# Performance work log

Hardware: AMD Instinct MI355X
Metric: run time of the kernel (lower is better)

## Reference

```python
import jax, jax.numpy as jnp
import numpy as np

SPATIAL_SHAPES = ((80, 80), (40, 40), (20, 20))  # strides 8/16/32 on 640x640
NUM_HEADS = 8
N_POINTS = 4
D_MODEL = 256
OFFSET_SCALE = 0.5
N_LEVELS = len(SPATIAL_SHAPES)
TOTAL_P = N_LEVELS * N_POINTS


def setup_inputs() -> dict:
    key = jax.random.key(0)
    ks = jax.random.split(key, 11)
    B, Q = 32, 300
    S = sum(h * w for h, w in SPATIAL_SHAPES)  # 8400
    d = D_MODEL
    s = 0.02
    return {
        "hidden_states": jax.random.normal(ks[0], (B, Q, d), jnp.float32),
        "encoder_hidden_states": jax.random.normal(ks[1], (B, S, d), jnp.float32),
        "reference_points": jax.random.uniform(ks[2], (B, Q, 1, 4), jnp.float32, 0.1, 0.9),
        "W_off": jax.random.normal(ks[3], (d, NUM_HEADS * TOTAL_P * 2), jnp.float32) * s,
        "b_off": jax.random.normal(ks[4], (NUM_HEADS * TOTAL_P * 2,), jnp.float32) * s,
        "W_attn": jax.random.normal(ks[5], (d, NUM_HEADS * TOTAL_P), jnp.float32) * s,
        "b_attn": jax.random.normal(ks[6], (NUM_HEADS * TOTAL_P,), jnp.float32) * s,
        "W_val": jax.random.normal(ks[7], (d, d), jnp.float32) * s,
        "b_val": jax.random.normal(ks[8], (d,), jnp.float32) * s,
        "W_out": jax.random.normal(ks[9], (d, d), jnp.float32) * s,
        "b_out": jax.random.normal(ks[10], (d,), jnp.float32) * s,
    }


def _bilinear_sample(img, grid):
    # img: (N, H, W, C); grid: (N, Q, P, 2), normalized coords in [-1, 1]
    # torch grid_sample(mode='bilinear', padding_mode='zeros', align_corners=False)
    N, Hh, Ww, C = img.shape
    gx = (grid[..., 0] + 1.0) * (Ww * 0.5) - 0.5
    gy = (grid[..., 1] + 1.0) * (Hh * 0.5) - 0.5
    x0 = jnp.floor(gx)
    y0 = jnp.floor(gy)
    wx1 = gx - x0
    wx0 = 1.0 - wx1
    wy1 = gy - y0
    wy0 = 1.0 - wy1
    n_idx = jnp.arange(N)[:, None, None]

    def tap(ix, iy, w):
        valid = (ix >= 0) & (ix < Ww) & (iy >= 0) & (iy < Hh)
        ixc = jnp.clip(ix, 0, Ww - 1).astype(jnp.int32)
        iyc = jnp.clip(iy, 0, Hh - 1).astype(jnp.int32)
        v = img[n_idx, iyc, ixc]  # (N, Q, P, C)
        return v * (w * valid.astype(w.dtype))[..., None]

    return (tap(x0, y0, wx0 * wy0) + tap(x0 + 1.0, y0, wx1 * wy0)
            + tap(x0, y0 + 1.0, wx0 * wy1) + tap(x0 + 1.0, y0 + 1.0, wx1 * wy1))


def reference(hidden_states, encoder_hidden_states, reference_points,
              W_off, b_off, W_attn, b_attn, W_val, b_val, W_out, b_out):
    B, Q, d = hidden_states.shape
    S = encoder_hidden_states.shape[1]
    H = NUM_HEADS
    C = d // H

    value = (encoder_hidden_states @ W_val + b_val).reshape(B, S, H, C)
    offs = (hidden_states @ W_off + b_off).reshape(B, Q, H, TOTAL_P, 2)
    attn = jax.nn.softmax((hidden_states @ W_attn + b_attn).reshape(B, Q, H, TOTAL_P), axis=-1)

    # 4-d reference points branch (boxes): loc = ref_xy + off * (1/P) * ref_wh * offset_scale
    n_points_scale = jnp.full((TOTAL_P, 1), 1.0 / N_POINTS, hidden_states.dtype)
    loc = (reference_points[:, :, None, :, :2]
           + offs * n_points_scale * reference_points[:, :, None, :, 2:] * OFFSET_SCALE)
    grids = 2.0 * loc - 1.0  # method='default'
    grids = grids.transpose(0, 2, 1, 3, 4).reshape(B * H, Q, TOTAL_P, 2)

    value_bh = value.transpose(0, 2, 1, 3).reshape(B * H, S, C)

    samples = []
    start = 0
    p0 = 0
    for (h, w) in SPATIAL_SHAPES:
        v_l = value_bh[:, start:start + h * w].reshape(B * H, h, w, C)
        g_l = grids[:, :, p0:p0 + N_POINTS]
        samples.append(_bilinear_sample(v_l, g_l))
        start += h * w
        p0 += N_POINTS
    sampled = jnp.concatenate(samples, axis=2)  # (B*H, Q, TOTAL_P, C)

    attn_bh = attn.transpose(0, 2, 1, 3).reshape(B * H, Q, TOTAL_P)
    out = jnp.einsum("nqpc,nqp->nqc", sampled, attn_bh)  # (B*H, Q, C)
    out = out.reshape(B, H, Q, C).transpose(0, 2, 1, 3).reshape(B, Q, H * C)
    return out @ W_out + b_out
```

## Files before the change

### kernel.cpp

```cpp
#include <hip/hip_runtime.h>
#include <hip/hip_fp16.h>

#define DEVI __device__ __forceinline__

typedef _Float16 f16x8 __attribute__((ext_vector_type(8)));
typedef float f32x4 __attribute__((ext_vector_type(4)));

static DEVI unsigned short f2h_u(float f) {
    _Float16 h = (_Float16)f;
    return __builtin_bit_cast(unsigned short, h);
}
static DEVI float h2f_u(unsigned short u) {
    return (float)__builtin_bit_cast(_Float16, u);
}
static DEVI unsigned pk2(float a, float b) {
    return (unsigned)f2h_u(a) | ((unsigned)f2h_u(b) << 16);
}


__global__ __launch_bounds__(256) void prep_weights(
    const float* __restrict__ W_val, const float* __restrict__ W_off,
    const float* __restrict__ W_attn, const float* __restrict__ W_out,
    const float* __restrict__ b_off, const float* __restrict__ b_attn,
    unsigned short* __restrict__ Wst, unsigned short* __restrict__ Wct,
    unsigned short* __restrict__ Wot, float* __restrict__ cbias)
{
    int idx = blockIdx.x * 256 + threadIdx.x;
    if (idx < 65536) {
        int n = idx >> 8, k = idx & 255;
        Wst[(((n >> 7) * 32 + (k >> 3)) * 128 + (n & 127)) * 8 + (k & 7)] =
            f2h_u(W_val[k * 256 + n]);
    } else if (idx < 65536 + 73728) {
        int j = idx - 65536;
        int n = j >> 8, k = j & 255;
        Wct[j] = f2h_u(n < 192 ? W_off[k * 192 + n] : W_attn[k * 96 + (n - 192)]);
    } else if (idx < 204800) {
        int j = idx - 139264;
        int n = j >> 8, k = j & 255;
        Wot[j] = f2h_u(W_out[k * 256 + n]);
    } else if (idx < 205088) {
        int j = idx - 204800;
        cbias[j] = (j < 192) ? b_off[j] : b_attn[j - 192];
    }
}

__global__ __launch_bounds__(256, 2) void gemm_value(
    const float* __restrict__ A, const unsigned short* __restrict__ Wst,
    const float* __restrict__ bias, unsigned short* __restrict__ out)
{
    __shared__ __align__(16) unsigned short Bs[32 * 128 * 8];
    const int tid  = threadIdx.x;
    const int wave = tid >> 6;
    const int lane = tid & 63;
    const int l15  = lane & 15;
    const int qd   = lane >> 4;
    const size_t m0 = (size_t)blockIdx.x * 64;

#pragma unroll
    for (int it = 0; it < 16; ++it) {
        const int c = wave * 16 + it;
        const unsigned short* gp = Wst + c * 512 + lane * 8;
        unsigned short* lp = Bs + c * 512;
        __builtin_amdgcn_global_load_lds(
            (const __attribute__((address_space(1))) void*)gp,
            (__attribute__((address_space(3))) void*)lp, 16, 0, 0);
    }

    const float* arow = A + (m0 + wave * 16 + l15) * 256 + qd * 8;
    float4 a0[8], a1[8];
#pragma unroll
    for (int kt = 0; kt < 8; ++kt) {
        a0[kt] = *(const float4*)(arow + kt * 32);
        a1[kt] = *(const float4*)(arow + kt * 32 + 4);
    }
    f16x8 af[8];
#pragma unroll
    for (int kt = 0; kt < 8; ++kt) {
        union { f16x8 v; uint4 u; } t;
        t.u.x = pk2(a0[kt].x, a0[kt].y);
        t.u.y = pk2(a0[kt].z, a0[kt].w);
        t.u.z = pk2(a1[kt].x, a1[kt].y);
        t.u.w = pk2(a1[kt].z, a1[kt].w);
        af[kt] = t.v;
    }

    f32x4 acc[2][8];
#pragma unroll
    for (int h = 0; h < 2; ++h)
#pragma unroll
        for (int i = 0; i < 8; ++i) acc[h][i] = (f32x4){0.f, 0.f, 0.f, 0.f};

    __syncthreads();

#pragma unroll
    for (int kt = 0; kt < 8; ++kt) {
#pragma unroll
        for (int ni = 0; ni < 8; ++ni) {
            f16x8 bf = *(const f16x8*)&Bs[(((kt * 4 + qd) * 128) + ni * 16 + l15) * 8];
            acc[0][ni] = __builtin_amdgcn_mfma_f32_16x16x32_f16(af[kt], bf, acc[0][ni], 0, 0, 0);
        }
    }
    __syncthreads();

#pragma unroll
    for (int it = 0; it < 16; ++it) {
        const int c = wave * 16 + it;
        const unsigned short* gp = Wst + 32768 + c * 512 + lane * 8;
        unsigned short* lp = Bs + c * 512;
        __builtin_amdgcn_global_load_lds(
            (const __attribute__((address_space(1))) void*)gp,
            (__attribute__((address_space(3))) void*)lp, 16, 0, 0);
    }
    __syncthreads();
#pragma unroll
    for (int kt = 0; kt < 8; ++kt) {
#pragma unroll
        for (int ni = 0; ni < 8; ++ni) {
            f16x8 bf = *(const f16x8*)&Bs[(((kt * 4 + qd) * 128) + ni * 16 + l15) * 8];
            acc[1][ni] = __builtin_amdgcn_mfma_f32_16x16x32_f16(af[kt], bf, acc[1][ni], 0, 0, 0);
        }
    }

    constexpr int LDH = 136;
#pragma unroll
    for (int h = 0; h < 2; ++h) {
        __syncthreads();
        unsigned short* Ch = Bs;
#pragma unroll
        for (int ni = 0; ni < 8; ++ni) {
            const float bb = bias[h * 128 + ni * 16 + l15];
#pragma unroll
            for (int r = 0; r < 4; ++r) {
                Ch[(wave * 16 + qd * 4 + r) * LDH + ni * 16 + l15] =
                    f2h_u(acc[h][ni][r] + bb);
            }
        }
        __syncthreads();
        for (int f = tid; f < 64 * 16; f += 256) {
            int row = f >> 4, c8 = f & 15;
            uint4 v = *(uint4*)&Ch[row * LDH + c8 * 8];
            *(uint4*)(out + (m0 + row) * 256 + h * 128 + c8 * 8) = v;
        }
    }
}

template<int BN>
__global__ __launch_bounds__(256) void gemm_f16(
    const float* __restrict__ A, const unsigned short* __restrict__ Wt,
    const float* __restrict__ bias, float* __restrict__ outp, int ldo)
{
    constexpr int NI  = BN / 16;
    constexpr int LDA = 40;
    constexpr int LDB = 40;
    constexpr int LDC = BN + 4;
    constexpr int SM1 = 64 * LDA * 2 + BN * LDB * 2;
    constexpr int SM2 = 64 * LDC * 4;
    constexpr int SMEM = SM1 > SM2 ? SM1 : SM2;
    __shared__ __align__(16) char smem[SMEM];
    unsigned short* As = (unsigned short*)smem;
    unsigned short* Bs = (unsigned short*)(smem + 64 * LDA * 2);
    float* Cs = (float*)smem;

    const int tid  = threadIdx.x;
    const int wave = tid >> 6;
    const int lane = tid & 63;
    const int l15  = lane & 15;
    const int qd   = lane >> 4;
    const int m0   = blockIdx.y * 64;
    const int n0   = blockIdx.x * BN;

    f32x4 acc[NI];
#pragma unroll
    for (int i = 0; i < NI; i++) acc[i] = (f32x4){0.f, 0.f, 0.f, 0.f};

#pragma unroll
    for (int kt = 0; kt < 8; kt++) {
#pragma unroll
        for (int i = 0; i < 2; i++) {
            int f = tid + i * 256;
            int row = f >> 3, c4 = f & 7;
            const float4 v = *(const float4*)(A + (size_t)(m0 + row) * 256 + kt * 32 + c4 * 4);
            uint2 p;
            p.x = pk2(v.x, v.y);
            p.y = pk2(v.z, v.w);
            *(uint2*)&As[row * LDA + c4 * 4] = p;
        }
        for (int f = tid; f < BN * 4; f += 256) {
            int row = f >> 2, ch = f & 3;
            uint4 v = *(const uint4*)(Wt + (size_t)(n0 + row) * 256 + kt * 32 + ch * 8);
            *(uint4*)&Bs[row * LDB + ch * 8] = v;
        }
        __syncthreads();
        f16x8 afr = *(const f16x8*)&As[(wave * 16 + l15) * LDA + qd * 8];
#pragma unroll
        for (int ni = 0; ni < NI; ni++) {
            f16x8 fb = *(const f16x8*)&Bs[(ni * 16 + l15) * LDB + qd * 8];
            acc[ni] = __builtin_amdgcn_mfma_f32_16x16x32_f16(afr, fb, acc[ni], 0, 0, 0);
        }
        __syncthreads();
    }

#pragma unroll
    for (int ni = 0; ni < NI; ni++) {
#pragma unroll
        for (int r = 0; r < 4; r++) {
            Cs[(wave * 16 + qd * 4 + r) * LDC + ni * 16 + l15] = acc[ni][r];
        }
    }
    __syncthreads();
    for (int f = tid; f < 64 * (BN / 4); f += 256) {
        int row = f / (BN / 4), c4 = f % (BN / 4);
        float4 v = *(const float4*)&Cs[row * LDC + c4 * 4];
        const float4 bb = *(const float4*)(bias + n0 + c4 * 4);
        v.x += bb.x; v.y += bb.y; v.z += bb.z; v.w += bb.w;
        *(float4*)(outp + (size_t)(m0 + row) * ldo + n0 + c4 * 4) = v;
    }
}

__global__ __launch_bounds__(256) void sample_attn(
    const float* __restrict__ P, const float* __restrict__ refp,
    const unsigned short* __restrict__ val, float* __restrict__ out_attn)
{
    __shared__ float sLoc[2][8][12][3];
    const int tid = threadIdx.x;
    const int rr  = tid >> 7;
    const int t   = tid & 127;
    const int row = blockIdx.x * 2 + rr;
    const int b   = row / 300;

    const float4 r4 = *(const float4*)(refp + (size_t)row * 4);

    if (t < 96) {
        const int h = t / 12, p = t - h * 12;
        const float* Pr = P + (size_t)row * 288;
        const float offx  = Pr[h * 24 + p * 2];
        const float offy  = Pr[h * 24 + p * 2 + 1];
        float m = -1e30f;
#pragma unroll
        for (int j = 0; j < 12; j++) m = fmaxf(m, Pr[192 + h * 12 + j]);
        float s = 0.f;
#pragma unroll
        for (int j = 0; j < 12; j++) s += expf(Pr[192 + h * 12 + j] - m);
        const float w = expf(Pr[192 + h * 12 + p] - m) / s;
        sLoc[rr][h][p][0] = r4.x + offx * 0.125f * r4.z;
        sLoc[rr][h][p][1] = r4.y + offy * 0.125f * r4.w;
        sLoc[rr][h][p][2] = w;
    }
    __syncthreads();

    const int hh = t >> 4;
    const int cp = t & 15;
    const unsigned short* vb = val + (size_t)b * 8400 * 256 + hh * 32 + cp * 2;
    float acc0 = 0.f, acc1 = 0.f;
#pragma unroll
    for (int p2 = 0; p2 < 12; p2++) {
        const int lvl  = p2 >> 2;
        const int W    = (lvl == 0) ? 80 : ((lvl == 1) ? 40 : 20);
        const int loff = (lvl == 0) ? 0 : ((lvl == 1) ? 6400 : 8000);
        const float lx = sLoc[rr][hh][p2][0];
        const float ly = sLoc[rr][hh][p2][1];
        const float w  = sLoc[rr][hh][p2][2];
        const float px = lx * (float)W - 0.5f;
        const float py = ly * (float)W - 0.5f;
        const float x0f = floorf(px), y0f = floorf(py);
        const float fx = px - x0f, fy = py - y0f;
        const int x0 = (int)x0f, y0 = (int)y0f;
        const int x1 = x0 + 1, y1 = y0 + 1;
        const float w00 = (1.f - fx) * (1.f - fy);
        const float w10 = fx * (1.f - fy);
        const float w01 = (1.f - fx) * fy;
        const float w11 = fx * fy;
        const bool vx0 = (x0 >= 0) && (x0 < W);
        const bool vx1 = (x1 >= 0) && (x1 < W);
        const bool vy0 = (y0 >= 0) && (y0 < W);
        const bool vy1 = (y1 >= 0) && (y1 < W);
        const int x0c = min(max(x0, 0), W - 1), x1c = min(max(x1, 0), W - 1);
        const int y0c = min(max(y0, 0), W - 1), y1c = min(max(y1, 0), W - 1);
        const unsigned u00 = *(const unsigned*)(vb + (size_t)(loff + y0c * W + x0c) * 256);
        const unsigned u10 = *(const unsigned*)(vb + (size_t)(loff + y0c * W + x1c) * 256);
        const unsigned u01 = *(const unsigned*)(vb + (size_t)(loff + y1c * W + x0c) * 256);
        const unsigned u11 = *(const unsigned*)(vb + (size_t)(loff + y1c * W + x1c) * 256);
        const float k00 = (vx0 && vy0) ? w00 : 0.f;
        const float k10 = (vx1 && vy0) ? w10 : 0.f;
        const float k01 = (vx0 && vy1) ? w01 : 0.f;
        const float k11 = (vx1 && vy1) ? w11 : 0.f;
        acc0 += w * (k00 * h2f_u(u00 & 0xffff) + k10 * h2f_u(u10 & 0xffff)
                   + k01 * h2f_u(u01 & 0xffff) + k11 * h2f_u(u11 & 0xffff));
        acc1 += w * (k00 * h2f_u(u00 >> 16) + k10 * h2f_u(u10 >> 16)
                   + k01 * h2f_u(u01 >> 16) + k11 * h2f_u(u11 >> 16));
    }
    float2 o; o.x = acc0; o.y = acc1;
    *(float2*)(out_attn + (size_t)row * 256 + hh * 32 + cp * 2) = o;
}

extern "C" void kernel_launch(void* const* d_in, const int* in_sizes, int n_in,
                              void* d_out, int out_size, void* d_ws, size_t ws_size,
                              hipStream_t stream)
{
    const float* hs     = (const float*)d_in[0];
    const float* enc    = (const float*)d_in[1];
    const float* refp   = (const float*)d_in[2];
    const float* W_off  = (const float*)d_in[3];
    const float* b_off  = (const float*)d_in[4];
    const float* W_attn = (const float*)d_in[5];
    const float* b_attn = (const float*)d_in[6];
    const float* W_val  = (const float*)d_in[7];
    const float* b_val  = (const float*)d_in[8];
    const float* W_out  = (const float*)d_in[9];
    const float* b_out  = (const float*)d_in[10];
    float* outp = (float*)d_out;

    char* ws = (char*)d_ws;
    unsigned short* val = (unsigned short*)ws;
    float* P            = (float*)(ws + 137625600);
    float* oattn        = (float*)(ws + 148684800);
    unsigned short* Wst = (unsigned short*)(ws + 158515200);
    unsigned short* Wct = (unsigned short*)(ws + 158646272);
    unsigned short* Wot = (unsigned short*)(ws + 158793728);
    float* cbias        = (float*)(ws + 158924800);

    prep_weights<<<802, 256, 0, stream>>>(W_val, W_off, W_attn, W_out,
                                          b_off, b_attn, Wst, Wct, Wot, cbias);
    gemm_f16<96><<<dim3(3, 150), 256, 0, stream>>>(hs, Wct, cbias, P, 288);
    gemm_value<<<4200, 256, 0, stream>>>(enc, Wst, b_val, val);
    sample_attn<<<4800, 256, 0, stream>>>(P, refp, val, oattn);
    gemm_f16<64><<<dim3(4, 150), 256, 0, stream>>>(oattn, Wot, b_out, outp, 256);
}
```

Measured before the change: 477.4 us.

## Restructure sampling kernel: XCD-aware batch mapping, wider loads, batched gathers

The sampling kernel now handles 4 query rows per block, and each thread covers 4 channels using 8-byte loads instead of 2. Block indices are remapped so each XCD works on whole batches, which keeps each batch's value tensor in a single L2. Offsets and weights for 6 points are computed first, then 24 gathers are issued together to expose memory-level parallelism. P rows are staged in shared memory and __expf is used for the softmax. The cost is higher register pressure from the gather arrays, and the XCD mapping assumes round-robin block dispatch.

```diff
diff --git a/kernel.cpp b/kernel.cpp
--- a/kernel.cpp
+++ b/kernel.cpp
@@ -221,76 +221,97 @@
     const float* __restrict__ P, const float* __restrict__ refp,
     const unsigned short* __restrict__ val, float* __restrict__ out_attn)
 {
-    __shared__ float sLoc[2][8][12][3];
-    const int tid = threadIdx.x;
-    const int rr  = tid >> 7;
-    const int t   = tid & 127;
-    const int row = blockIdx.x * 2 + rr;
-    const int b   = row / 300;
-
-    const float4 r4 = *(const float4*)(refp + (size_t)row * 4);
-
-    if (t < 96) {
-        const int h = t / 12, p = t - h * 12;
-        const float* Pr = P + (size_t)row * 288;
-        const float offx  = Pr[h * 24 + p * 2];
-        const float offy  = Pr[h * 24 + p * 2 + 1];
+    __shared__ float sP[1152];
+    __shared__ float sLoc[4][8][12][3];
+    const int tid   = threadIdx.x;
+    const int blk   = blockIdx.x;
+    const int xcd   = blk & 7;
+    const int local = blk >> 3;
+    const int b     = xcd + 8 * (local / 75);
+    const int q0    = (local % 75) * 4;
+    const int row0  = b * 300 + q0;
+
+    {
+        const float4* src = (const float4*)(P + (size_t)row0 * 288);
+        for (int f = tid; f < 288; f += 256) ((float4*)sP)[f] = src[f];
+    }
+    __syncthreads();
+
+    for (int j = tid; j < 384; j += 256) {
+        const int r = j / 96, rem = j - r * 96;
+        const int h = rem / 12, p = rem - h * 12;
+        const float* Pr = sP + r * 288;
+        const float* Lg = Pr + 192 + h * 12;
         float m = -1e30f;
 #pragma unroll
-        for (int j = 0; j < 12; j++) m = fmaxf(m, Pr[192 + h * 12 + j]);
+        for (int jj = 0; jj < 12; jj++) m = fmaxf(m, Lg[jj]);
         float s = 0.f;
 #pragma unroll
-        for (int j = 0; j < 12; j++) s += expf(Pr[192 + h * 12 + j] - m);
-        const float w = expf(Pr[192 + h * 12 + p] - m) / s;
-        sLoc[rr][h][p][0] = r4.x + offx * 0.125f * r4.z;
-        sLoc[rr][h][p][1] = r4.y + offy * 0.125f * r4.w;
-        sLoc[rr][h][p][2] = w;
-    }
-    __syncthreads();
-
-    const int hh = t >> 4;
-    const int cp = t & 15;
-    const unsigned short* vb = val + (size_t)b * 8400 * 256 + hh * 32 + cp * 2;
-    float acc0 = 0.f, acc1 = 0.f;
-#pragma unroll
-    for (int p2 = 0; p2 < 12; p2++) {
-        const int lvl  = p2 >> 2;
-        const int W    = (lvl == 0) ? 80 : ((lvl == 1) ? 40 : 20);
-        const int loff = (lvl == 0) ? 0 : ((lvl == 1) ? 6400 : 8000);
-        const float lx = sLoc[rr][hh][p2][0];
-        const float ly = sLoc[rr][hh][p2][1];
-        const float w  = sLoc[rr][hh][p2][2];
-        const float px = lx * (float)W - 0.5f;
-        const float py = ly * (float)W - 0.5f;
-        const float x0f = floorf(px), y0f = floorf(py);
-        const float fx = px - x0f, fy = py - y0f;
-        const int x0 = (int)x0f, y0 = (int)y0f;
-        const int x1 = x0 + 1, y1 = y0 + 1;
-        const float w00 = (1.f - fx) * (1.f - fy);
-        const float w10 = fx * (1.f - fy);
-        const float w01 = (1.f - fx) * fy;
-        const float w11 = fx * fy;
-        const bool vx0 = (x0 >= 0) && (x0 < W);
-        const bool vx1 = (x1 >= 0) && (x1 < W);
-        const bool vy0 = (y0 >= 0) && (y0 < W);
-        const bool vy1 = (y1 >= 0) && (y1 < W);
-        const int x0c = min(max(x0, 0), W - 1), x1c = min(max(x1, 0), W - 1);
-        const int y0c = min(max(y0, 0), W - 1), y1c = min(max(y1, 0), W - 1);
-        const unsigned u00 = *(const unsigned*)(vb + (size_t)(loff + y0c * W + x0c) * 256);
-        const unsigned u10 = *(const unsigned*)(vb + (size_t)(loff + y0c * W + x1c) * 256);
-        const unsigned u01 = *(const unsigned*)(vb + (size_t)(loff + y1c * W + x0c) * 256);
-        const unsigned u11 = *(const unsigned*)(vb + (size_t)(loff + y1c * W + x1c) * 256);
-        const float k00 = (vx0 && vy0) ? w00 : 0.f;
-        const float k10 = (vx1 && vy0) ? w10 : 0.f;
-        const float k01 = (vx0 && vy1) ? w01 : 0.f;
-        const float k11 = (vx1 && vy1) ? w11 : 0.f;
-        acc0 += w * (k00 * h2f_u(u00 & 0xffff) + k10 * h2f_u(u10 & 0xffff)
-                   + k01 * h2f_u(u01 & 0xffff) + k11 * h2f_u(u11 & 0xffff));
-        acc1 += w * (k00 * h2f_u(u00 >> 16) + k10 * h2f_u(u10 >> 16)
-                   + k01 * h2f_u(u01 >> 16) + k11 * h2f_u(u11 >> 16));
-    }
-    float2 o; o.x = acc0; o.y = acc1;
-    *(float2*)(out_attn + (size_t)row * 256 + hh * 32 + cp * 2) = o;
+        for (int jj = 0; jj < 12; jj++) s += __expf(Lg[jj] - m);
+        const float w = __expf(Lg[p] - m) / s;
+        const float4 r4 = *(const float4*)(refp + (size_t)(row0 + r) * 4);
+        sLoc[r][h][p][0] = r4.x + Pr[h * 24 + p * 2]     * 0.125f * r4.z;
+        sLoc[r][h][p][1] = r4.y + Pr[h * 24 + p * 2 + 1] * 0.125f * r4.w;
+        sLoc[r][h][p][2] = w;
+    }
+    __syncthreads();
+
+    const int r  = tid >> 6;
+    const int t6 = tid & 63;
+    const int h  = t6 >> 3;
+    const int l8 = t6 & 7;
+    const int row = row0 + r;
+    const unsigned short* vb = val + (size_t)b * 8400 * 256 + h * 32 + l8 * 4;
+
+    float a0 = 0.f, a1 = 0.f, a2 = 0.f, a3 = 0.f;
+#pragma unroll
+    for (int half = 0; half < 2; ++half) {
+        int   off[24];
+        float kw[24];
+#pragma unroll
+        for (int pp = 0; pp < 6; ++pp) {
+            const int p2   = half * 6 + pp;
+            const int lvl  = p2 >> 2;
+            const int W    = (lvl == 0) ? 80 : ((lvl == 1) ? 40 : 20);
+            const int loff = (lvl == 0) ? 0 : ((lvl == 1) ? 6400 : 8000);
+            const float lx = sLoc[r][h][p2][0];
+            const float ly = sLoc[r][h][p2][1];
+            const float w  = sLoc[r][h][p2][2];
+            const float px = lx * (float)W - 0.5f;
+            const float py = ly * (float)W - 0.5f;
+            const float x0f = floorf(px), y0f = floorf(py);
+            const float fx = px - x0f, fy = py - y0f;
+            const int x0 = (int)x0f, y0 = (int)y0f;
+            const int x1 = x0 + 1, y1 = y0 + 1;
+            const bool vx0 = (x0 >= 0) && (x0 < W);
+            const bool vx1 = (x1 >= 0) && (x1 < W);
+            const bool vy0 = (y0 >= 0) && (y0 < W);
+            const bool vy1 = (y1 >= 0) && (y1 < W);
+            const int x0c = min(max(x0, 0), W - 1), x1c = min(max(x1, 0), W - 1);
+            const int y0c = min(max(y0, 0), W - 1), y1c = min(max(y1, 0), W - 1);
+            kw[pp * 4 + 0] = (vx0 && vy0) ? w * (1.f - fx) * (1.f - fy) : 0.f;
+            kw[pp * 4 + 1] = (vx1 && vy0) ? w * fx * (1.f - fy) : 0.f;
+            kw[pp * 4 + 2] = (vx0 && vy1) ? w * (1.f - fx) * fy : 0.f;
+            kw[pp * 4 + 3] = (vx1 && vy1) ? w * fx * fy : 0.f;
+            off[pp * 4 + 0] = (loff + y0c * W + x0c) * 256;
+            off[pp * 4 + 1] = (loff + y0c * W + x1c) * 256;
+            off[pp * 4 + 2] = (loff + y1c * W + x0c) * 256;
+            off[pp * 4 + 3] = (loff + y1c * W + x1c) * 256;
+        }
+        uint2 u[24];
+#pragma unroll
+        for (int t = 0; t < 24; ++t) u[t] = *(const uint2*)(vb + off[t]);
+#pragma unroll
+        for (int t = 0; t < 24; ++t) {
+            const float k = kw[t];
+            a0 = fmaf(k, h2f_u(u[t].x & 0xffff), a0);
+            a1 = fmaf(k, h2f_u(u[t].x >> 16),    a1);
+            a2 = fmaf(k, h2f_u(u[t].y & 0xffff), a2);
+            a3 = fmaf(k, h2f_u(u[t].y >> 16),    a3);
+        }
+    }
+    float4 o; o.x = a0; o.y = a1; o.z = a2; o.w = a3;
+    *(float4*)(out_attn + (size_t)row * 256 + h * 32 + l8 * 4) = o;
 }
 
 extern "C" void kernel_launch(void* const* d_in, const int* in_sizes, int n_in,
@@ -323,6 +344,6 @@
                                           b_off, b_attn, Wst, Wct, Wot, cbias);
     gemm_f16<96><<<dim3(3, 150), 256, 0, stream>>>(hs, Wct, cbias, P, 288);
     gemm_value<<<4200, 256, 0, stream>>>(enc, Wst, b_val, val);
-    sample_attn<<<4800, 256, 0, stream>>>(P, refp, val, oattn);
+    sample_attn<<<2400, 256, 0, stream>>>(P, refp, val, oattn);
     gemm_f16<64><<<dim3(4, 150), 256, 0, stream>>>(oattn, Wot, b_out, outp, 256);
 }
```

New measurement: 476.6 us. About the same (-0.2%).
